# Optimization experiments

Measured on AMD Instinct MI355X. Metric: run time of the kernel, lower is better.

The kernel has to match this reference:

```python
import jax, jax.numpy as jnp
from jax import lax
import numpy as np

B, T, I, H, C = 4096, 2048, 1, 16, 2


def setup_inputs() -> dict:
    key = jax.random.key(0)
    ks = jax.random.split(key, 7)
    return {
        "x": jax.random.normal(ks[0], (B, T, I), dtype=jnp.float32),
        "W_ih": jax.random.normal(ks[1], (H, I), dtype=jnp.float32) * (1.0 / np.sqrt(H)),
        "b_ih": jax.random.normal(ks[2], (H,), dtype=jnp.float32) * (1.0 / np.sqrt(H)),
        "W_hh": jax.random.normal(ks[3], (H, H), dtype=jnp.float32) * (1.0 / np.sqrt(H)),
        "b_hh": jax.random.normal(ks[4], (H,), dtype=jnp.float32) * (1.0 / np.sqrt(H)),
        "W_fc": jax.random.normal(ks[5], (C, H), dtype=jnp.float32) * (1.0 / np.sqrt(H)),
        "b_fc": jax.random.normal(ks[6], (C,), dtype=jnp.float32) * (1.0 / np.sqrt(H)),
    }


def reference(x, W_ih, b_ih, W_hh, b_hh, W_fc, b_fc):
    # Precompute input contribution for all timesteps: [B, T, H]
    xi = jnp.einsum('bti,hi->bth', x, W_ih) + b_ih
    h0 = jnp.zeros((x.shape[0], W_hh.shape[0]), dtype=x.dtype)

    def step(h, xt):
        # PyTorch RNN cell (relu): h_t = relu(W_ih x_t + b_ih + W_hh h_{t-1} + b_hh)
        h = jax.nn.relu(xt + h @ W_hh.T + b_hh)
        return h, None

    hT, _ = lax.scan(step, h0, jnp.swapaxes(xi, 0, 1))  # scan over T
    # fc applied to the last timestep's hidden state (out[:, -1, :] == hT)
    return hT @ W_fc.T + b_fc
```

## Files before the change

kernel.cpp:

```cpp
#include <hip/hip_runtime.h>

#define T_LEN 2048

typedef float f4 __attribute__((ext_vector_type(4)));

__device__ __forceinline__ void step(float& h, float xs, const float (&w)[16],
                                     float wih, float bias) {
  float a0, a1, a2, a3;
  asm("v_fma_f32 %0, %5, %6, %7\n\t"
      "v_fmac_f32 %0, %4, %8\n\t"
      "v_mul_f32_dpp %1, %4, %9  row_ror:1  row_mask:0xf bank_mask:0xf\n\t"
      "v_mul_f32_dpp %2, %4, %10 row_ror:2  row_mask:0xf bank_mask:0xf\n\t"
      "v_mul_f32_dpp %3, %4, %11 row_ror:3  row_mask:0xf bank_mask:0xf\n\t"
      "v_fmac_f32_dpp %0, %4, %12 row_ror:4  row_mask:0xf bank_mask:0xf\n\t"
      "v_fmac_f32_dpp %1, %4, %13 row_ror:5  row_mask:0xf bank_mask:0xf\n\t"
      "v_fmac_f32_dpp %2, %4, %14 row_ror:6  row_mask:0xf bank_mask:0xf\n\t"
      "v_fmac_f32_dpp %3, %4, %15 row_ror:7  row_mask:0xf bank_mask:0xf\n\t"
      "v_fmac_f32_dpp %0, %4, %16 row_ror:8  row_mask:0xf bank_mask:0xf\n\t"
      "v_fmac_f32_dpp %1, %4, %17 row_ror:9  row_mask:0xf bank_mask:0xf\n\t"
      "v_fmac_f32_dpp %2, %4, %18 row_ror:10 row_mask:0xf bank_mask:0xf\n\t"
      "v_fmac_f32_dpp %3, %4, %19 row_ror:11 row_mask:0xf bank_mask:0xf\n\t"
      "v_fmac_f32_dpp %0, %4, %20 row_ror:12 row_mask:0xf bank_mask:0xf\n\t"
      "v_fmac_f32_dpp %1, %4, %21 row_ror:13 row_mask:0xf bank_mask:0xf\n\t"
      "v_fmac_f32_dpp %2, %4, %22 row_ror:14 row_mask:0xf bank_mask:0xf\n\t"
      "v_fmac_f32_dpp %3, %4, %23 row_ror:15 row_mask:0xf bank_mask:0xf\n\t"
      "v_add_f32 %0, %0, %1\n\t"
      "v_add_f32 %2, %2, %3\n\t"
      "v_add_f32 %0, %0, %2\n\t"
      "v_max_f32 %4, 0, %0"
      : "=&v"(a0), "=&v"(a1), "=&v"(a2), "=&v"(a3), "+v"(h)
      : "v"(xs), "v"(wih), "v"(bias),
        "v"(w[0]), "v"(w[1]), "v"(w[2]), "v"(w[3]),
        "v"(w[4]), "v"(w[5]), "v"(w[6]), "v"(w[7]),
        "v"(w[8]), "v"(w[9]), "v"(w[10]), "v"(w[11]),
        "v"(w[12]), "v"(w[13]), "v"(w[14]), "v"(w[15]));
}

__global__ __launch_bounds__(256) void rnn_relu_kernel(
    const float* __restrict__ x, const float* __restrict__ W_ih,
    const float* __restrict__ b_ih, const float* __restrict__ W_hh,
    const float* __restrict__ b_hh, const float* __restrict__ W_fc,
    const float* __restrict__ b_fc, float* __restrict__ out) {
  const int tid = threadIdx.x;
  const int j   = tid & 15;
  const int b   = blockIdx.x * 16 + (tid >> 4);

  int pr = __builtin_amdgcn_update_dpp(0, j, 0x121, 0xF, 0xF, true);
  const bool plus = (pr == ((j + 1) & 15));

  float w[16];
#pragma unroll
  for (int s = 0; s < 16; ++s) {
    int k = (j + (plus ? s : (16 - s))) & 15;
    w[s] = W_hh[j * 16 + k];
  }
  const float wih  = W_ih[j];
  const float bias = b_ih[j] + b_hh[j];

  const f4* __restrict__ xr = (const f4*)(x + (size_t)b * T_LEN);

  float h = 0.0f;
  f4 c0 = xr[0], c1 = xr[1], c2 = xr[2], c3 = xr[3];

#pragma unroll 1
  for (int t0 = 0; t0 < T_LEN; t0 += 16) {
    f4 n0 = {0,0,0,0}, n1 = {0,0,0,0}, n2 = {0,0,0,0}, n3 = {0,0,0,0};
    if (t0 + 16 < T_LEN) {
      const f4* p = xr + ((t0 + 16) >> 2);
      n0 = p[0]; n1 = p[1]; n2 = p[2]; n3 = p[3];
    }
    step(h, c0.x, w, wih, bias);
    step(h, c0.y, w, wih, bias);
    step(h, c0.z, w, wih, bias);
    step(h, c0.w, w, wih, bias);
    step(h, c1.x, w, wih, bias);
    step(h, c1.y, w, wih, bias);
    step(h, c1.z, w, wih, bias);
    step(h, c1.w, w, wih, bias);
    step(h, c2.x, w, wih, bias);
    step(h, c2.y, w, wih, bias);
    step(h, c2.z, w, wih, bias);
    step(h, c2.w, w, wih, bias);
    step(h, c3.x, w, wih, bias);
    step(h, c3.y, w, wih, bias);
    step(h, c3.z, w, wih, bias);
    step(h, c3.w, w, wih, bias);
    c0 = n0; c1 = n1; c2 = n2; c3 = n3;
  }

  float p0 = h * W_fc[j];
  float p1 = h * W_fc[16 + j];
  p0 += __int_as_float(__builtin_amdgcn_ds_swizzle(__float_as_int(p0), 0x041F));
  p1 += __int_as_float(__builtin_amdgcn_ds_swizzle(__float_as_int(p1), 0x041F));
  p0 += __int_as_float(__builtin_amdgcn_ds_swizzle(__float_as_int(p0), 0x081F));
  p1 += __int_as_float(__builtin_amdgcn_ds_swizzle(__float_as_int(p1), 0x081F));
  p0 += __int_as_float(__builtin_amdgcn_ds_swizzle(__float_as_int(p0), 0x101F));
  p1 += __int_as_float(__builtin_amdgcn_ds_swizzle(__float_as_int(p1), 0x101F));
  p0 += __int_as_float(__builtin_amdgcn_ds_swizzle(__float_as_int(p0), 0x201F));
  p1 += __int_as_float(__builtin_amdgcn_ds_swizzle(__float_as_int(p1), 0x201F));

  if (j == 0) {
    out[b * 2 + 0] = p0 + b_fc[0];
    out[b * 2 + 1] = p1 + b_fc[1];
  }
}

extern "C" void kernel_launch(void* const* d_in, const int* in_sizes, int n_in,
                              void* d_out, int out_size, void* d_ws, size_t ws_size,
                              hipStream_t stream) {
  const float* x    = (const float*)d_in[0];
  const float* W_ih = (const float*)d_in[1];
  const float* b_ih = (const float*)d_in[2];
  const float* W_hh = (const float*)d_in[3];
  const float* b_hh = (const float*)d_in[4];
  const float* W_fc = (const float*)d_in[5];
  const float* b_fc = (const float*)d_in[6];
  float* out = (float*)d_out;

  const int B = 4096;
  dim3 grid(B / 16);
  dim3 block(256);
  hipLaunchKernelGGL(rnn_relu_kernel, grid, block, 0, stream,
                     x, W_ih, b_ih, W_hh, b_hh, W_fc, b_fc, out);
}
```

Measured before the change: 109.0 us.

## Split each hidden-state dot product across wave halves with permlane32 swap

Each batch row's 16-wide matvec is now split over two 32-lane halves of the wave, each doing 8 DPP-rotated FMAs, and the partial sums are combined with permlane32_swap. This halves the dependent FMA chain per timestep to shorten the serial recurrence latency. It doubles the thread count (grid doubled) and adds a row_ror:8 DPP and a cross-half swap per step. The conditional prefetch is also made branchless by wrapping the index.

Result: slower. 141.6 us (+29.9%).

```diff
diff --git a/kernel.cpp b/kernel.cpp
--- a/kernel.cpp
+++ b/kernel.cpp
@@ -3,37 +3,32 @@
 #define T_LEN 2048
 
 typedef float f4 __attribute__((ext_vector_type(4)));
+typedef unsigned int u32x2 __attribute__((ext_vector_type(2)));
 
-__device__ __forceinline__ void step(float& h, float xs, const float (&w)[16],
-                                     float wih, float bias) {
-  float a0, a1, a2, a3;
-  asm("v_fma_f32 %0, %5, %6, %7\n\t"
-      "v_fmac_f32 %0, %4, %8\n\t"
-      "v_mul_f32_dpp %1, %4, %9  row_ror:1  row_mask:0xf bank_mask:0xf\n\t"
-      "v_mul_f32_dpp %2, %4, %10 row_ror:2  row_mask:0xf bank_mask:0xf\n\t"
-      "v_mul_f32_dpp %3, %4, %11 row_ror:3  row_mask:0xf bank_mask:0xf\n\t"
-      "v_fmac_f32_dpp %0, %4, %12 row_ror:4  row_mask:0xf bank_mask:0xf\n\t"
-      "v_fmac_f32_dpp %1, %4, %13 row_ror:5  row_mask:0xf bank_mask:0xf\n\t"
-      "v_fmac_f32_dpp %2, %4, %14 row_ror:6  row_mask:0xf bank_mask:0xf\n\t"
-      "v_fmac_f32_dpp %3, %4, %15 row_ror:7  row_mask:0xf bank_mask:0xf\n\t"
-      "v_fmac_f32_dpp %0, %4, %16 row_ror:8  row_mask:0xf bank_mask:0xf\n\t"
-      "v_fmac_f32_dpp %1, %4, %17 row_ror:9  row_mask:0xf bank_mask:0xf\n\t"
-      "v_fmac_f32_dpp %2, %4, %18 row_ror:10 row_mask:0xf bank_mask:0xf\n\t"
-      "v_fmac_f32_dpp %3, %4, %19 row_ror:11 row_mask:0xf bank_mask:0xf\n\t"
-      "v_fmac_f32_dpp %0, %4, %20 row_ror:12 row_mask:0xf bank_mask:0xf\n\t"
-      "v_fmac_f32_dpp %1, %4, %21 row_ror:13 row_mask:0xf bank_mask:0xf\n\t"
-      "v_fmac_f32_dpp %2, %4, %22 row_ror:14 row_mask:0xf bank_mask:0xf\n\t"
-      "v_fmac_f32_dpp %3, %4, %23 row_ror:15 row_mask:0xf bank_mask:0xf\n\t"
-      "v_add_f32 %0, %0, %1\n\t"
-      "v_add_f32 %2, %2, %3\n\t"
-      "v_add_f32 %0, %0, %2\n\t"
-      "v_max_f32 %4, 0, %0"
-      : "=&v"(a0), "=&v"(a1), "=&v"(a2), "=&v"(a3), "+v"(h)
-      : "v"(xs), "v"(wih), "v"(bias),
-        "v"(w[0]), "v"(w[1]), "v"(w[2]), "v"(w[3]),
-        "v"(w[4]), "v"(w[5]), "v"(w[6]), "v"(w[7]),
-        "v"(w[8]), "v"(w[9]), "v"(w[10]), "v"(w[11]),
-        "v"(w[12]), "v"(w[13]), "v"(w[14]), "v"(w[15]));
+__device__ __forceinline__ float stepk(float h, float xs, const float (&w)[8],
+                                       float wih_e, float bias_e, bool hi) {
+  int h8 = __builtin_amdgcn_update_dpp(0, __float_as_int(h), 0x128, 0xF, 0xF, true);
+  float hs = hi ? __int_as_float(h8) : h;
+
+  float a0, a1;
+  asm("v_fma_f32      %0, %[xs], %[wih], %[bs]\n\t"
+      "v_fmac_f32     %0, %[hs], %[w0]\n\t"
+      "v_mul_f32_dpp  %1, %[hs], %[w1] row_ror:1 row_mask:0xf bank_mask:0xf\n\t"
+      "v_fmac_f32_dpp %0, %[hs], %[w2] row_ror:2 row_mask:0xf bank_mask:0xf\n\t"
+      "v_fmac_f32_dpp %1, %[hs], %[w3] row_ror:3 row_mask:0xf bank_mask:0xf\n\t"
+      "v_fmac_f32_dpp %0, %[hs], %[w4] row_ror:4 row_mask:0xf bank_mask:0xf\n\t"
+      "v_fmac_f32_dpp %1, %[hs], %[w5] row_ror:5 row_mask:0xf bank_mask:0xf\n\t"
+      "v_fmac_f32_dpp %0, %[hs], %[w6] row_ror:6 row_mask:0xf bank_mask:0xf\n\t"
+      "v_fmac_f32_dpp %1, %[hs], %[w7] row_ror:7 row_mask:0xf bank_mask:0xf\n\t"
+      "v_add_f32      %0, %0, %1"
+      : "=&v"(a0), "=&v"(a1)
+      : [xs]"v"(xs), [wih]"v"(wih_e), [bs]"v"(bias_e), [hs]"v"(hs),
+        [w0]"v"(w[0]), [w1]"v"(w[1]), [w2]"v"(w[2]), [w3]"v"(w[3]),
+        [w4]"v"(w[4]), [w5]"v"(w[5]), [w6]"v"(w[6]), [w7]"v"(w[7]));
+
+  u32x2 r = __builtin_amdgcn_permlane32_swap(__float_as_uint(a0),
+                                             __float_as_uint(a0), false, false);
+  return fmaxf(__uint_as_float(r[0]) + __uint_as_float(r[1]), 0.0f);
 }
 
 __global__ __launch_bounds__(256) void rnn_relu_kernel(
@@ -41,21 +36,23 @@
     const float* __restrict__ b_ih, const float* __restrict__ W_hh,
     const float* __restrict__ b_hh, const float* __restrict__ W_fc,
     const float* __restrict__ b_fc, float* __restrict__ out) {
-  const int tid = threadIdx.x;
-  const int j   = tid & 15;
-  const int b   = blockIdx.x * 16 + (tid >> 4);
+  const int tid  = threadIdx.x;
+  const int gtid = blockIdx.x * 256 + tid;
+  const int j    = tid & 15;
+  const bool hi  = (tid & 32) != 0;
+  const int b    = (gtid >> 6) * 2 + ((tid >> 4) & 1);
 
   int pr = __builtin_amdgcn_update_dpp(0, j, 0x121, 0xF, 0xF, true);
   const bool plus = (pr == ((j + 1) & 15));
 
-  float w[16];
+  float w[8];
 #pragma unroll
-  for (int s = 0; s < 16; ++s) {
-    int k = (j + (plus ? s : (16 - s))) & 15;
+  for (int s = 0; s < 8; ++s) {
+    int k = (j + (plus ? s : (16 - s) & 15) + (hi ? 8 : 0)) & 15;
     w[s] = W_hh[j * 16 + k];
   }
-  const float wih  = W_ih[j];
-  const float bias = b_ih[j] + b_hh[j];
+  const float wih_e  = hi ? 0.0f : W_ih[j];
+  const float bias_e = hi ? 0.0f : (b_ih[j] + b_hh[j]);
 
   const f4* __restrict__ xr = (const f4*)(x + (size_t)b * T_LEN);
 
@@ -64,27 +61,25 @@
 
 #pragma unroll 1
   for (int t0 = 0; t0 < T_LEN; t0 += 16) {
-    f4 n0 = {0,0,0,0}, n1 = {0,0,0,0}, n2 = {0,0,0,0}, n3 = {0,0,0,0};
-    if (t0 + 16 < T_LEN) {
-      const f4* p = xr + ((t0 + 16) >> 2);
-      n0 = p[0]; n1 = p[1]; n2 = p[2]; n3 = p[3];
-    }
-    step(h, c0.x, w, wih, bias);
-    step(h, c0.y, w, wih, bias);
-    step(h, c0.z, w, wih, bias);
-    step(h, c0.w, w, wih, bias);
-    step(h, c1.x, w, wih, bias);
-    step(h, c1.y, w, wih, bias);
-    step(h, c1.z, w, wih, bias);
-    step(h, c1.w, w, wih, bias);
-    step(h, c2.x, w, wih, bias);
-    step(h, c2.y, w, wih, bias);
-    step(h, c2.z, w, wih, bias);
-    step(h, c2.w, w, wih, bias);
-    step(h, c3.x, w, wih, bias);
-    step(h, c3.y, w, wih, bias);
-    step(h, c3.z, w, wih, bias);
-    step(h, c3.w, w, wih, bias);
+    const int tn = (t0 + 16) & (T_LEN - 1);
+    const f4* p = xr + (tn >> 2);
+    f4 n0 = p[0], n1 = p[1], n2 = p[2], n3 = p[3];
+    h = stepk(h, c0.x, w, wih_e, bias_e, hi);
+    h = stepk(h, c0.y, w, wih_e, bias_e, hi);
+    h = stepk(h, c0.z, w, wih_e, bias_e, hi);
+    h = stepk(h, c0.w, w, wih_e, bias_e, hi);
+    h = stepk(h, c1.x, w, wih_e, bias_e, hi);
+    h = stepk(h, c1.y, w, wih_e, bias_e, hi);
+    h = stepk(h, c1.z, w, wih_e, bias_e, hi);
+    h = stepk(h, c1.w, w, wih_e, bias_e, hi);
+    h = stepk(h, c2.x, w, wih_e, bias_e, hi);
+    h = stepk(h, c2.y, w, wih_e, bias_e, hi);
+    h = stepk(h, c2.z, w, wih_e, bias_e, hi);
+    h = stepk(h, c2.w, w, wih_e, bias_e, hi);
+    h = stepk(h, c3.x, w, wih_e, bias_e, hi);
+    h = stepk(h, c3.y, w, wih_e, bias_e, hi);
+    h = stepk(h, c3.z, w, wih_e, bias_e, hi);
+    h = stepk(h, c3.w, w, wih_e, bias_e, hi);
     c0 = n0; c1 = n1; c2 = n2; c3 = n3;
   }
 
@@ -99,7 +94,7 @@
   p0 += __int_as_float(__builtin_amdgcn_ds_swizzle(__float_as_int(p0), 0x201F));
   p1 += __int_as_float(__builtin_amdgcn_ds_swizzle(__float_as_int(p1), 0x201F));
 
-  if (j == 0) {
+  if ((tid & 47) == 0) {
     out[b * 2 + 0] = p0 + b_fc[0];
     out[b * 2 + 1] = p1 + b_fc[1];
   }
@@ -118,7 +113,7 @@
   float* out = (float*)d_out;
 
   const int B = 4096;
-  dim3 grid(B / 16);
+  dim3 grid(B / 8);
   dim3 block(256);
   hipLaunchKernelGGL(rnn_relu_kernel, grid, block, 0, stream,
                      x, W_ih, b_ih, W_hh, b_hh, W_fc, b_fc, out);
```

## Software-pipeline input projection one chunk ahead and deepen prefetch to 32 steps

Applied to the files above, without the earlier changes.

Each step's input projection (x*W_ih + bias) is now computed for the next 32-step chunk inside the step asm, off the dependent chain, so the recurrence FMA starts directly from a precomputed value. Input loads are double-buffered in 32-step halves, with the clamped final prefetch reading valid memory instead of using a branch. The launch bound is set to one block per CU minimum, allowing more registers. This removes one dependent FMA per step from the serial critical path, at the cost of higher register pressure.

Measured after the change: 103.2 us. 5.3% less time.

```diff
diff --git a/kernel.cpp b/kernel.cpp
--- a/kernel.cpp
+++ b/kernel.cpp
@@ -4,39 +4,54 @@
 
 typedef float f4 __attribute__((ext_vector_type(4)));
 
-__device__ __forceinline__ void step(float& h, float xs, const float (&w)[16],
-                                     float wih, float bias) {
+__device__ __forceinline__ void step(float& h, float xi, float raw, float& xo,
+                                     const float (&w)[16], float wih, float bias) {
   float a0, a1, a2, a3;
-  asm("v_fma_f32 %0, %5, %6, %7\n\t"
-      "v_fmac_f32 %0, %4, %8\n\t"
-      "v_mul_f32_dpp %1, %4, %9  row_ror:1  row_mask:0xf bank_mask:0xf\n\t"
-      "v_mul_f32_dpp %2, %4, %10 row_ror:2  row_mask:0xf bank_mask:0xf\n\t"
-      "v_mul_f32_dpp %3, %4, %11 row_ror:3  row_mask:0xf bank_mask:0xf\n\t"
-      "v_fmac_f32_dpp %0, %4, %12 row_ror:4  row_mask:0xf bank_mask:0xf\n\t"
-      "v_fmac_f32_dpp %1, %4, %13 row_ror:5  row_mask:0xf bank_mask:0xf\n\t"
-      "v_fmac_f32_dpp %2, %4, %14 row_ror:6  row_mask:0xf bank_mask:0xf\n\t"
-      "v_fmac_f32_dpp %3, %4, %15 row_ror:7  row_mask:0xf bank_mask:0xf\n\t"
-      "v_fmac_f32_dpp %0, %4, %16 row_ror:8  row_mask:0xf bank_mask:0xf\n\t"
-      "v_fmac_f32_dpp %1, %4, %17 row_ror:9  row_mask:0xf bank_mask:0xf\n\t"
-      "v_fmac_f32_dpp %2, %4, %18 row_ror:10 row_mask:0xf bank_mask:0xf\n\t"
-      "v_fmac_f32_dpp %3, %4, %19 row_ror:11 row_mask:0xf bank_mask:0xf\n\t"
-      "v_fmac_f32_dpp %0, %4, %20 row_ror:12 row_mask:0xf bank_mask:0xf\n\t"
-      "v_fmac_f32_dpp %1, %4, %21 row_ror:13 row_mask:0xf bank_mask:0xf\n\t"
-      "v_fmac_f32_dpp %2, %4, %22 row_ror:14 row_mask:0xf bank_mask:0xf\n\t"
-      "v_fmac_f32_dpp %3, %4, %23 row_ror:15 row_mask:0xf bank_mask:0xf\n\t"
-      "v_add_f32 %0, %0, %1\n\t"
-      "v_add_f32 %2, %2, %3\n\t"
-      "v_add_f32 %0, %0, %2\n\t"
-      "v_max_f32 %4, 0, %0"
-      : "=&v"(a0), "=&v"(a1), "=&v"(a2), "=&v"(a3), "+v"(h)
-      : "v"(xs), "v"(wih), "v"(bias),
-        "v"(w[0]), "v"(w[1]), "v"(w[2]), "v"(w[3]),
-        "v"(w[4]), "v"(w[5]), "v"(w[6]), "v"(w[7]),
-        "v"(w[8]), "v"(w[9]), "v"(w[10]), "v"(w[11]),
-        "v"(w[12]), "v"(w[13]), "v"(w[14]), "v"(w[15]));
+  asm("v_fma_f32 %[xo], %[raw], %[wih], %[bs]\n\t"
+      "v_fma_f32 %[a0], %[h], %[w0], %[xi]\n\t"
+      "v_mul_f32_dpp  %[a1], %[h], %[w1]  row_ror:1  row_mask:0xf bank_mask:0xf\n\t"
+      "v_mul_f32_dpp  %[a2], %[h], %[w2]  row_ror:2  row_mask:0xf bank_mask:0xf\n\t"
+      "v_mul_f32_dpp  %[a3], %[h], %[w3]  row_ror:3  row_mask:0xf bank_mask:0xf\n\t"
+      "v_fmac_f32_dpp %[a0], %[h], %[w4]  row_ror:4  row_mask:0xf bank_mask:0xf\n\t"
+      "v_fmac_f32_dpp %[a1], %[h], %[w5]  row_ror:5  row_mask:0xf bank_mask:0xf\n\t"
+      "v_fmac_f32_dpp %[a2], %[h], %[w6]  row_ror:6  row_mask:0xf bank_mask:0xf\n\t"
+      "v_fmac_f32_dpp %[a3], %[h], %[w7]  row_ror:7  row_mask:0xf bank_mask:0xf\n\t"
+      "v_fmac_f32_dpp %[a0], %[h], %[w8]  row_ror:8  row_mask:0xf bank_mask:0xf\n\t"
+      "v_fmac_f32_dpp %[a1], %[h], %[w9]  row_ror:9  row_mask:0xf bank_mask:0xf\n\t"
+      "v_fmac_f32_dpp %[a2], %[h], %[w10] row_ror:10 row_mask:0xf bank_mask:0xf\n\t"
+      "v_fmac_f32_dpp %[a3], %[h], %[w11] row_ror:11 row_mask:0xf bank_mask:0xf\n\t"
+      "v_fmac_f32_dpp %[a0], %[h], %[w12] row_ror:12 row_mask:0xf bank_mask:0xf\n\t"
+      "v_fmac_f32_dpp %[a1], %[h], %[w13] row_ror:13 row_mask:0xf bank_mask:0xf\n\t"
+      "v_fmac_f32_dpp %[a2], %[h], %[w14] row_ror:14 row_mask:0xf bank_mask:0xf\n\t"
+      "v_fmac_f32_dpp %[a3], %[h], %[w15] row_ror:15 row_mask:0xf bank_mask:0xf\n\t"
+      "v_add_f32 %[a0], %[a0], %[a1]\n\t"
+      "v_add_f32 %[a2], %[a2], %[a3]\n\t"
+      "v_add_f32 %[a0], %[a0], %[a2]\n\t"
+      "v_max_f32 %[h], 0, %[a0]"
+      : [a0] "=&v"(a0), [a1] "=&v"(a1), [a2] "=&v"(a2), [a3] "=&v"(a3),
+        [xo] "=&v"(xo), [h] "+v"(h)
+      : [xi] "v"(xi), [raw] "v"(raw), [wih] "v"(wih), [bs] "v"(bias),
+        [w0] "v"(w[0]),  [w1] "v"(w[1]),  [w2] "v"(w[2]),  [w3] "v"(w[3]),
+        [w4] "v"(w[4]),  [w5] "v"(w[5]),  [w6] "v"(w[6]),  [w7] "v"(w[7]),
+        [w8] "v"(w[8]),  [w9] "v"(w[9]),  [w10] "v"(w[10]), [w11] "v"(w[11]),
+        [w12] "v"(w[12]), [w13] "v"(w[13]), [w14] "v"(w[14]), [w15] "v"(w[15]));
 }
 
-__global__ __launch_bounds__(256) void rnn_relu_kernel(
+#define Q4(XI, RQ, XO, q)                          \
+  step(h, XI[4*(q)+0], RQ[q].x, XO[4*(q)+0], w, wih, bias); \
+  step(h, XI[4*(q)+1], RQ[q].y, XO[4*(q)+1], w, wih, bias); \
+  step(h, XI[4*(q)+2], RQ[q].z, XO[4*(q)+2], w, wih, bias); \
+  step(h, XI[4*(q)+3], RQ[q].w, XO[4*(q)+3], w, wih, bias);
+
+#define HALF(XI, RQ, XO) \
+  Q4(XI, RQ, XO, 0) Q4(XI, RQ, XO, 1) Q4(XI, RQ, XO, 2) Q4(XI, RQ, XO, 3) \
+  Q4(XI, RQ, XO, 4) Q4(XI, RQ, XO, 5) Q4(XI, RQ, XO, 6) Q4(XI, RQ, XO, 7)
+
+#define LD8(R, PS) \
+  R[0] = (PS)[0]; R[1] = (PS)[1]; R[2] = (PS)[2]; R[3] = (PS)[3]; \
+  R[4] = (PS)[4]; R[5] = (PS)[5]; R[6] = (PS)[6]; R[7] = (PS)[7];
+
+__global__ __launch_bounds__(256, 1) void rnn_relu_kernel(
     const float* __restrict__ x, const float* __restrict__ W_ih,
     const float* __restrict__ b_ih, const float* __restrict__ W_hh,
     const float* __restrict__ b_hh, const float* __restrict__ W_fc,
@@ -59,33 +74,30 @@
 
   const f4* __restrict__ xr = (const f4*)(x + (size_t)b * T_LEN);
 
+  f4 RA[8], RB[8];
+  float XA[32], XB[32];
+  LD8(RA, xr)
+  LD8(RB, xr + 8)
+#pragma unroll
+  for (int i = 0; i < 8; ++i) {
+    XA[4*i+0] = fmaf(RA[i].x, wih, bias);
+    XA[4*i+1] = fmaf(RA[i].y, wih, bias);
+    XA[4*i+2] = fmaf(RA[i].z, wih, bias);
+    XA[4*i+3] = fmaf(RA[i].w, wih, bias);
+  }
+
   float h = 0.0f;
-  f4 c0 = xr[0], c1 = xr[1], c2 = xr[2], c3 = xr[3];
+  const f4* p2 = xr + 16;
 
 #pragma unroll 1
-  for (int t0 = 0; t0 < T_LEN; t0 += 16) {
-    f4 n0 = {0,0,0,0}, n1 = {0,0,0,0}, n2 = {0,0,0,0}, n3 = {0,0,0,0};
-    if (t0 + 16 < T_LEN) {
-      const f4* p = xr + ((t0 + 16) >> 2);
-      n0 = p[0]; n1 = p[1]; n2 = p[2]; n3 = p[3];
-    }
-    step(h, c0.x, w, wih, bias);
-    step(h, c0.y, w, wih, bias);
-    step(h, c0.z, w, wih, bias);
-    step(h, c0.w, w, wih, bias);
-    step(h, c1.x, w, wih, bias);
-    step(h, c1.y, w, wih, bias);
-    step(h, c1.z, w, wih, bias);
-    step(h, c1.w, w, wih, bias);
-    step(h, c2.x, w, wih, bias);
-    step(h, c2.y, w, wih, bias);
-    step(h, c2.z, w, wih, bias);
-    step(h, c2.w, w, wih, bias);
-    step(h, c3.x, w, wih, bias);
-    step(h, c3.y, w, wih, bias);
-    step(h, c3.z, w, wih, bias);
-    step(h, c3.w, w, wih, bias);
-    c0 = n0; c1 = n1; c2 = n2; c3 = n3;
+  for (int k = 0; k < 64; k += 2) {
+    const f4* psA = (k + 2 < 64) ? p2 : xr;
+    LD8(RA, psA)
+    HALF(XA, RB, XB)
+    const f4* psB = (k + 3 < 64) ? (p2 + 8) : xr;
+    LD8(RB, psB)
+    HALF(XB, RA, XA)
+    p2 += 16;
   }
 
   float p0 = h * W_fc[j];
```
